# Kernel optimization log

Hardware: AMD Instinct MI355X
Metric: run time of the kernel (lower is better)

Reference implementation:

```python
import jax, jax.numpy as jnp
import numpy as np

K_TOP = 16
SPLITS = 16


def setup_inputs() -> dict:
    key = jax.random.key(0)
    kq, kt = jax.random.split(key)
    queries = jax.random.normal(kq, (4096, 128), dtype=jnp.float32)
    table = jax.random.normal(kt, (4096, 128, 128), dtype=jnp.float32)
    return {"queries": queries, "table": table}


def reference(queries, table):
    n_queries, vector_dim = queries.shape
    rows, scores_per_row, _ = table.shape
    table_size = rows * scores_per_row
    queries_per_split = n_queries // SPLITS
    q_split = queries.reshape(SPLITS, queries_per_split, vector_dim)
    row_offsets = jnp.arange(0, table_size, scores_per_row)  # [rows]

    def split_top_k(split_queries):
        # scores: [q, rows, values_per_row]
        split_scores = jnp.einsum('qd,rvd->qrv', split_queries, table)
        top_id_by_row = jnp.argmax(split_scores, axis=-1)        # [q, rows]
        top_score_by_row = jnp.max(split_scores, axis=-1)        # [q, rows]
        # top-k rows by per-row max score (descending)
        top_row_idx = jnp.argsort(top_score_by_row, axis=-1)[:, :-K_TOP - 1:-1]  # [q, k]
        # matmul_slice == gather along axis -1 (one-hot matmul trick on TPU)
        ids_by_topk_row = jnp.take_along_axis(top_id_by_row, top_row_idx, axis=-1)  # [q, k]
        split_topk_values = table[top_row_idx, ids_by_topk_row]  # [q, k, d]
        top_table_id_by_row = top_id_by_row + row_offsets        # [q, rows]
        split_topk_ids = jnp.take_along_axis(top_table_id_by_row, top_row_idx, axis=-1)
        split_topk_scores = jnp.take_along_axis(top_score_by_row, top_row_idx, axis=-1)
        return split_topk_values, split_topk_scores, split_topk_ids

    topk_values, topk_scores, topk_ids = jax.lax.map(split_top_k, q_split)
    topk_values = topk_values.reshape(n_queries, K_TOP, -1)
    topk_scores = topk_scores.reshape(n_queries, K_TOP)
    topk_ids = topk_ids.reshape(n_queries, K_TOP)
    return topk_values, topk_scores, topk_ids
```

## Files before the change

kernel.cpp:

```cpp
#include <hip/hip_runtime.h>
#include <stdint.h>


typedef __attribute__((ext_vector_type(8))) short short8;
typedef __attribute__((ext_vector_type(4))) float floatx4;
typedef __attribute__((ext_vector_type(16))) float floatx16;
typedef unsigned long long u64;
typedef unsigned int u32;

#define NQ 4096
#define NR 4096
#define NV 128
#define ND 128
#define KTOP 16
#define RC 16
#define NCHUNK (NR / RC)
#define CPC 8
#define CSEL 24
#define BCAP 1024

__device__ __forceinline__ unsigned short f2bf(float f) {
  u32 u = __float_as_uint(f);
  u32 r = u + 0x7FFFu + ((u >> 16) & 1u);
  return (unsigned short)(r >> 16);
}
__device__ __forceinline__ u32 key_of(float s) {
  u32 b = __float_as_uint(s);
  return (b & 0x80000000u) ? ~b : (b | 0x80000000u);
}
__device__ __forceinline__ float unkey(u32 k) {
  u32 b = (k & 0x80000000u) ? (k & 0x7FFFFFFFu) : ~k;
  return __uint_as_float(b);
}
__device__ __forceinline__ void glds16(const void* g, void* l) {
  __builtin_amdgcn_global_load_lds(
      (const __attribute__((address_space(1))) unsigned int*)g,
      (__attribute__((address_space(3))) unsigned int*)l, 16, 0, 0);
}

__global__ void k0_convert(const float* __restrict__ t, unsigned short* __restrict__ o) {
  size_t i = ((size_t)blockIdx.x * 256 + threadIdx.x) * 4;
  float4 v = *reinterpret_cast<const float4*>(t + i);
  ushort4 r;
  r.x = f2bf(v.x); r.y = f2bf(v.y); r.z = f2bf(v.z); r.w = f2bf(v.w);
  *reinterpret_cast<ushort4*>(o + i) = r;
}

__launch_bounds__(256, 2)
__global__ void k1_coarse(const float* __restrict__ Q, const unsigned short* __restrict__ T16,
                          u64* __restrict__ cand) {
  __shared__ short Blds[2][128 * 128];

  const int tid = threadIdx.x;
  const int wave = tid >> 6;
  const int lane = tid & 63;
  const int l31 = lane & 31;
  const int l15 = lane & 15;
  const int half = lane >> 5;
  const int qblock = blockIdx.x;
  const int chunk = blockIdx.y;

  short8 bfrag[8];
  {
    const float* qp = Q + (size_t)(qblock * 128 + wave * 32 + l31) * 128;
#pragma unroll
    for (int kb = 0; kb < 8; kb++) {
      float4 x = *reinterpret_cast<const float4*>(qp + kb * 16 + half * 8);
      float4 y = *reinterpret_cast<const float4*>(qp + kb * 16 + half * 8 + 4);
      short8 b;
      b[0] = (short)f2bf(x.x); b[1] = (short)f2bf(x.y);
      b[2] = (short)f2bf(x.z); b[3] = (short)f2bf(x.w);
      b[4] = (short)f2bf(y.x); b[5] = (short)f2bf(y.y);
      b[6] = (short)f2bf(y.z); b[7] = (short)f2bf(y.w);
      bfrag[kb] = b;
    }
  }

  int goff[8];
#pragma unroll
  for (int i = 0; i < 8; i++) {
    int v = wave * 32 + i * 4 + (lane >> 4);
    int kb = l15 ^ (v & 15);
    goff[i] = v * 256 + kb * 16;
  }
  const char* chunkbase = (const char*)(T16 + (size_t)(chunk * RC) * (NV * ND));

#pragma unroll
  for (int i = 0; i < 8; i++)
    glds16(chunkbase + goff[i], &Blds[0][(wave * 8 + i) * 512 + lane * 8]);
  __syncthreads();

  u64 a[CPC];
#pragma unroll
  for (int i = 0; i < CPC; i++) a[i] = 0;

  const short* abase = &Blds[0][l31 * 128];
  for (int rl = 0; rl < RC; rl++) {
    const int cur = rl & 1;
    if (rl < RC - 1) {
      const char* rs = chunkbase + (size_t)(rl + 1) * 32768;
#pragma unroll
      for (int i = 0; i < 8; i++)
        glds16(rs + goff[i], &Blds[1 - cur][(wave * 8 + i) * 512 + lane * 8]);
    }

    float run = -3.402823466e+38f;
#pragma unroll
    for (int t = 0; t < 4; t++) {
      floatx16 acc = 0;
#pragma unroll
      for (int kb = 0; kb < 8; kb++) {
        const short* ap = abase + cur * 16384 + t * 4096 +
                          8 * ((kb * 2 + half) ^ (l31 & 15));
        short8 af = *reinterpret_cast<const short8*>(ap);
        acc = __builtin_amdgcn_mfma_f32_32x32x16_bf16(af, bfrag[kb], acc, 0, 0, 0);
      }
      float m = acc[0];
#pragma unroll
      for (int r = 1; r < 16; r++) m = fmaxf(m, acc[r]);
      run = fmaxf(run, m);
    }
    run = fmaxf(run, __shfl_xor(run, 32, 64));

    u64 x = ((u64)key_of(run) << 32) | (u32)(chunk * RC + rl);
    if (x > a[CPC - 1]) {
#pragma unroll
      for (int p = 0; p < CPC; p++) {
        u64 mx = a[p] > x ? a[p] : x;
        u64 mn = a[p] > x ? x : a[p];
        a[p] = mx; x = mn;
      }
    }
    __syncthreads();
  }

  if (lane < 32) {
    const int q = qblock * 128 + wave * 32 + l31;
    u64* dst = cand + (size_t)q * (NCHUNK * CPC) + chunk * CPC;
#pragma unroll
    for (int i = 0; i < CPC; i++) dst[i] = a[i];
  }
}

__global__ void k2_select(const u64* __restrict__ cand, u64* __restrict__ refined,
                          u32* __restrict__ cnt, u32* __restrict__ bucket) {
  const int q = blockIdx.x;
  const int lane = threadIdx.x;
  const u64* base = cand + (size_t)q * (NCHUNK * CPC);
  u64 a[12];
#pragma unroll
  for (int i = 0; i < 12; i++) a[i] = 0;
  for (int i = 0; i < 32; i++) {
    u64 x = base[i * 64 + lane];
    if (x > a[11]) {
#pragma unroll
      for (int p = 0; p < 12; p++) {
        u64 mx = a[p] > x ? a[p] : x;
        u64 mn = a[p] > x ? x : a[p];
        a[p] = mx; x = mn;
      }
    }
  }
  if (lane < CSEL) refined[(size_t)q * CSEL + lane] = 0;

  for (int j = 0; j < CSEL; j++) {
    u64 head = a[0];
    u64 W = head;
#pragma unroll
    for (int off = 1; off < 64; off <<= 1) {
      u64 o = __shfl_xor(W, off, 64);
      if (o > W) W = o;
    }
    if (head == W) {
#pragma unroll
      for (int p = 0; p < 11; p++) a[p] = a[p + 1];
      a[11] = 0;
      u32 row = (u32)W & 4095u;
      u32 slot = atomicAdd(cnt + row, 1u);
      if (slot < BCAP) bucket[(size_t)row * BCAP + slot] = ((u32)q << 5) | (u32)j;
    }
  }
}

__global__ void k3_refine(const float* __restrict__ Q, const float* __restrict__ table,
                          const u32* __restrict__ cnt, const u32* __restrict__ bucket,
                          u64* __restrict__ refined) {
  __shared__ float rowv[128 * 128];
  const int row = blockIdx.x;
  const int tid = threadIdx.x;
  u32 n = cnt[row];
  if (n > BCAP) n = BCAP;
  if (n == 0) return;
  const float* src = table + (size_t)row * (NV * ND);
#pragma unroll
  for (int i = 0; i < 8; i++) {
    int idx = i * 2048 + tid * 4;
    int v = idx >> 7;
    int d4 = tid & 31;
    *reinterpret_cast<float4*>(&rowv[v * 128 + ((d4 ^ (v & 31)) << 2)]) =
        *reinterpret_cast<const float4*>(src + idx);
  }
  __syncthreads();
  const int v = tid & 127;
  const int lane = tid & 63;
  const int sw = v & 31;
  for (u32 ei = (u32)(tid >> 7); ei < n; ei += 4) {
    u32 ent = __builtin_amdgcn_readfirstlane(bucket[(size_t)row * BCAP + ei]);
    u32 q = ent >> 5, j = ent & 31u;
    const float* qp = Q + (size_t)q * 128;
    float acc = 0.f;
#pragma unroll
    for (int d4 = 0; d4 < 32; d4++) {
      float4 rv = *reinterpret_cast<const float4*>(&rowv[v * 128 + ((d4 ^ sw) << 2)]);
      acc = fmaf(rv.x, qp[d4 * 4 + 0], acc);
      acc = fmaf(rv.y, qp[d4 * 4 + 1], acc);
      acc = fmaf(rv.z, qp[d4 * 4 + 2], acc);
      acc = fmaf(rv.w, qp[d4 * 4 + 3], acc);
    }
    u64 p = ((u64)key_of(acc) << 32) | (u32)(127 - v);
#pragma unroll
    for (int off = 1; off < 64; off <<= 1) {
      u64 o = __shfl_xor(p, off, 64);
      if (o > p) p = o;
    }
    if (lane == 0) {
      u32 vbest = 127u - (u32)(p & 0xFFFFFFFFu);
      u64 packed = ((p >> 32) << 32) | (u32)(row * 128 + vbest);
      atomicMax(reinterpret_cast<unsigned long long*>(&refined[(size_t)q * CSEL + j]), packed);
    }
  }
}

__global__ void k4_finalize(const float* __restrict__ table, const u64* __restrict__ refined,
                            float* __restrict__ out) {
  __shared__ u64 arr[CSEL];
  __shared__ u32 fids[KTOP];
  __shared__ float scs[KTOP];
  const int q = blockIdx.x;
  const int tid = threadIdx.x;
  if (tid < CSEL) arr[tid] = refined[(size_t)q * CSEL + tid];
  __syncthreads();
  if (tid == 0) {
    for (int i = 1; i < CSEL; i++) {
      u64 x = arr[i]; int p = i;
      while (p > 0 && arr[p - 1] < x) { arr[p] = arr[p - 1]; p--; }
      arr[p] = x;
    }
    for (int i = 0; i < KTOP; i++) {
      fids[i] = (u32)arr[i];
      scs[i] = unkey((u32)(arr[i] >> 32));
    }
  }
  __syncthreads();
  const int i = tid >> 4, sub = tid & 15;
  const float* src = table + (size_t)fids[i] * 128 + sub * 8;
  float* dst = out + ((size_t)q * KTOP + i) * 128 + sub * 8;
  *reinterpret_cast<float4*>(dst) = *reinterpret_cast<const float4*>(src);
  *reinterpret_cast<float4*>(dst + 4) = *reinterpret_cast<const float4*>(src + 4);
  if (tid < KTOP) {
    out[8388608 + (size_t)q * KTOP + tid] = scs[tid];
    out[8388608 + 65536 + (size_t)q * KTOP + tid] = (float)fids[tid];
  }
}

extern "C" void kernel_launch(void* const* d_in, const int* in_sizes, int n_in,
                              void* d_out, int out_size, void* d_ws, size_t ws_size,
                              hipStream_t stream) {
  (void)in_sizes; (void)n_in; (void)out_size; (void)ws_size;
  const float* Q = (const float*)d_in[0];
  const float* T = (const float*)d_in[1];
  float* out = (float*)d_out;
  char* ws = (char*)d_ws;
  unsigned short* T16 = (unsigned short*)ws;
  u64* cand    = (u64*)(ws + 134217728);
  u32* cnt     = (u32*)(ws + 134217728 + 67108864);
  u32* bucket  = (u32*)(ws + 134217728 + 67108864 + 16384);
  u64* refined = (u64*)(ws + 134217728 + 67108864 + 16384 + 16777216);

  hipMemsetAsync(cnt, 0, NR * sizeof(u32), stream);
  k0_convert<<<65536, 256, 0, stream>>>(T, T16);
  k1_coarse<<<dim3(32, 256), 256, 0, stream>>>(Q, T16, cand);
  k2_select<<<NQ, 64, 0, stream>>>(cand, refined, cnt, bucket);
  k3_refine<<<NR, 512, 0, stream>>>(Q, T, cnt, bucket, refined);
  k4_finalize<<<NQ, 256, 0, stream>>>(T, refined, out);
}
```

Before: 1.211 ms.

## Double queries per wave in coarse kernel and batch four entries in refine

```diff
diff --git a/kernel.cpp b/kernel.cpp
--- a/kernel.cpp
+++ b/kernel.cpp
@@ -37,6 +37,23 @@
       (const __attribute__((address_space(1))) unsigned int*)g,
       (__attribute__((address_space(3))) unsigned int*)l, 16, 0, 0);
 }
+__device__ __forceinline__ float max16(floatx16 a) {
+  float m0 = fmaxf(fmaxf(a[0], a[1]), fmaxf(a[2], a[3]));
+  float m1 = fmaxf(fmaxf(a[4], a[5]), fmaxf(a[6], a[7]));
+  float m2 = fmaxf(fmaxf(a[8], a[9]), fmaxf(a[10], a[11]));
+  float m3 = fmaxf(fmaxf(a[12], a[13]), fmaxf(a[14], a[15]));
+  return fmaxf(fmaxf(m0, m1), fmaxf(m2, m3));
+}
+__device__ __forceinline__ void insert8(u64* a, u64 x) {
+  if (x > a[CPC - 1]) {
+#pragma unroll
+    for (int p = 0; p < CPC; p++) {
+      u64 mx = a[p] > x ? a[p] : x;
+      u64 mn = a[p] > x ? x : a[p];
+      a[p] = mx; x = mn;
+    }
+  }
+}
 
 __global__ void k0_convert(const float* __restrict__ t, unsigned short* __restrict__ o) {
   size_t i = ((size_t)blockIdx.x * 256 + threadIdx.x) * 4;
@@ -60,19 +77,27 @@
   const int qblock = blockIdx.x;
   const int chunk = blockIdx.y;
 
-  short8 bfrag[8];
+  short8 bf0[8], bf1[8];
   {
-    const float* qp = Q + (size_t)(qblock * 128 + wave * 32 + l31) * 128;
+    const float* qp0 = Q + (size_t)(qblock * 256 + wave * 64 + l31) * 128;
+    const float* qp1 = qp0 + 32 * 128;
 #pragma unroll
     for (int kb = 0; kb < 8; kb++) {
-      float4 x = *reinterpret_cast<const float4*>(qp + kb * 16 + half * 8);
-      float4 y = *reinterpret_cast<const float4*>(qp + kb * 16 + half * 8 + 4);
+      float4 x = *reinterpret_cast<const float4*>(qp0 + kb * 16 + half * 8);
+      float4 y = *reinterpret_cast<const float4*>(qp0 + kb * 16 + half * 8 + 4);
       short8 b;
       b[0] = (short)f2bf(x.x); b[1] = (short)f2bf(x.y);
       b[2] = (short)f2bf(x.z); b[3] = (short)f2bf(x.w);
       b[4] = (short)f2bf(y.x); b[5] = (short)f2bf(y.y);
       b[6] = (short)f2bf(y.z); b[7] = (short)f2bf(y.w);
-      bfrag[kb] = b;
+      bf0[kb] = b;
+      x = *reinterpret_cast<const float4*>(qp1 + kb * 16 + half * 8);
+      y = *reinterpret_cast<const float4*>(qp1 + kb * 16 + half * 8 + 4);
+      b[0] = (short)f2bf(x.x); b[1] = (short)f2bf(x.y);
+      b[2] = (short)f2bf(x.z); b[3] = (short)f2bf(x.w);
+      b[4] = (short)f2bf(y.x); b[5] = (short)f2bf(y.y);
+      b[6] = (short)f2bf(y.z); b[7] = (short)f2bf(y.w);
+      bf1[kb] = b;
     }
   }
 
@@ -90,9 +115,9 @@
     glds16(chunkbase + goff[i], &Blds[0][(wave * 8 + i) * 512 + lane * 8]);
   __syncthreads();
 
-  u64 a[CPC];
-#pragma unroll
-  for (int i = 0; i < CPC; i++) a[i] = 0;
+  u64 a0[CPC], a1[CPC];
+#pragma unroll
+  for (int i = 0; i < CPC; i++) { a0[i] = 0; a1[i] = 0; }
 
   const short* abase = &Blds[0][l31 * 128];
   for (int rl = 0; rl < RC; rl++) {
@@ -104,41 +129,36 @@
         glds16(rs + goff[i], &Blds[1 - cur][(wave * 8 + i) * 512 + lane * 8]);
     }
 
-    float run = -3.402823466e+38f;
+    float run0 = -3.402823466e+38f, run1 = -3.402823466e+38f;
 #pragma unroll
     for (int t = 0; t < 4; t++) {
-      floatx16 acc = 0;
+      floatx16 acc0 = 0, acc1 = 0;
 #pragma unroll
       for (int kb = 0; kb < 8; kb++) {
         const short* ap = abase + cur * 16384 + t * 4096 +
                           8 * ((kb * 2 + half) ^ (l31 & 15));
         short8 af = *reinterpret_cast<const short8*>(ap);
-        acc = __builtin_amdgcn_mfma_f32_32x32x16_bf16(af, bfrag[kb], acc, 0, 0, 0);
+        acc0 = __builtin_amdgcn_mfma_f32_32x32x16_bf16(af, bf0[kb], acc0, 0, 0, 0);
+        acc1 = __builtin_amdgcn_mfma_f32_32x32x16_bf16(af, bf1[kb], acc1, 0, 0, 0);
       }
-      float m = acc[0];
-#pragma unroll
-      for (int r = 1; r < 16; r++) m = fmaxf(m, acc[r]);
-      run = fmaxf(run, m);
-    }
-    run = fmaxf(run, __shfl_xor(run, 32, 64));
-
-    u64 x = ((u64)key_of(run) << 32) | (u32)(chunk * RC + rl);
-    if (x > a[CPC - 1]) {
-#pragma unroll
-      for (int p = 0; p < CPC; p++) {
-        u64 mx = a[p] > x ? a[p] : x;
-        u64 mn = a[p] > x ? x : a[p];
-        a[p] = mx; x = mn;
-      }
-    }
+      run0 = fmaxf(run0, max16(acc0));
+      run1 = fmaxf(run1, max16(acc1));
+    }
+    run0 = fmaxf(run0, __shfl_xor(run0, 32, 64));
+    run1 = fmaxf(run1, __shfl_xor(run1, 32, 64));
+
+    u32 rid = (u32)(chunk * RC + rl);
+    insert8(a0, ((u64)key_of(run0) << 32) | rid);
+    insert8(a1, ((u64)key_of(run1) << 32) | rid);
     __syncthreads();
   }
 
   if (lane < 32) {
-    const int q = qblock * 128 + wave * 32 + l31;
-    u64* dst = cand + (size_t)q * (NCHUNK * CPC) + chunk * CPC;
-#pragma unroll
-    for (int i = 0; i < CPC; i++) dst[i] = a[i];
+    const int q0 = qblock * 256 + wave * 64 + l31;
+    u64* dst0 = cand + (size_t)q0 * (NCHUNK * CPC) + chunk * CPC;
+    u64* dst1 = dst0 + (size_t)32 * (NCHUNK * CPC);
+#pragma unroll
+    for (int i = 0; i < CPC; i++) { dst0[i] = a0[i]; dst1[i] = a1[i]; }
   }
 }
 
@@ -179,6 +199,22 @@
       u32 slot = atomicAdd(cnt + row, 1u);
       if (slot < BCAP) bucket[(size_t)row * BCAP + slot] = ((u32)q << 5) | (u32)j;
     }
+  }
+}
+
+__device__ __forceinline__ void k3_emit(float acc, u32 ent, int row, int v, int lane,
+                                        u64* __restrict__ refined) {
+  u64 p = ((u64)key_of(acc) << 32) | (u32)(127 - v);
+#pragma unroll
+  for (int off = 1; off < 64; off <<= 1) {
+    u64 o = __shfl_xor(p, off, 64);
+    if (o > p) p = o;
+  }
+  if (lane == 0) {
+    u32 q = ent >> 5, j = ent & 31u;
+    u32 vbest = 127u - (u32)(p & 0xFFFFFFFFu);
+    u64 packed = ((p >> 32) << 32) | (u32)(row * 128 + vbest);
+    atomicMax(reinterpret_cast<unsigned long long*>(&refined[(size_t)q * CSEL + j]), packed);
   }
 }
 
@@ -193,41 +229,53 @@
   if (n == 0) return;
   const float* src = table + (size_t)row * (NV * ND);
 #pragma unroll
-  for (int i = 0; i < 8; i++) {
-    int idx = i * 2048 + tid * 4;
+  for (int i = 0; i < 16; i++) {
+    int idx = i * 1024 + tid * 4;
     int v = idx >> 7;
     int d4 = tid & 31;
     *reinterpret_cast<float4*>(&rowv[v * 128 + ((d4 ^ (v & 31)) << 2)]) =
         *reinterpret_cast<const float4*>(src + idx);
   }
   __syncthreads();
+  const int g = tid >> 7;
   const int v = tid & 127;
   const int lane = tid & 63;
   const int sw = v & 31;
-  for (u32 ei = (u32)(tid >> 7); ei < n; ei += 4) {
-    u32 ent = __builtin_amdgcn_readfirstlane(bucket[(size_t)row * BCAP + ei]);
-    u32 q = ent >> 5, j = ent & 31u;
-    const float* qp = Q + (size_t)q * 128;
-    float acc = 0.f;
+  const u32* bk = bucket + (size_t)row * BCAP;
+  for (u32 e0 = (u32)(g * 4); e0 < n; e0 += 8) {
+    u32 ent0 = __builtin_amdgcn_readfirstlane(bk[e0]);
+    u32 ent1 = __builtin_amdgcn_readfirstlane(bk[e0 + 1 < n ? e0 + 1 : e0]);
+    u32 ent2 = __builtin_amdgcn_readfirstlane(bk[e0 + 2 < n ? e0 + 2 : e0]);
+    u32 ent3 = __builtin_amdgcn_readfirstlane(bk[e0 + 3 < n ? e0 + 3 : e0]);
+    const float* qp0 = Q + (size_t)(ent0 >> 5) * 128;
+    const float* qp1 = Q + (size_t)(ent1 >> 5) * 128;
+    const float* qp2 = Q + (size_t)(ent2 >> 5) * 128;
+    const float* qp3 = Q + (size_t)(ent3 >> 5) * 128;
+    float c0 = 0.f, c1 = 0.f, c2 = 0.f, c3 = 0.f;
 #pragma unroll
     for (int d4 = 0; d4 < 32; d4++) {
       float4 rv = *reinterpret_cast<const float4*>(&rowv[v * 128 + ((d4 ^ sw) << 2)]);
-      acc = fmaf(rv.x, qp[d4 * 4 + 0], acc);
-      acc = fmaf(rv.y, qp[d4 * 4 + 1], acc);
-      acc = fmaf(rv.z, qp[d4 * 4 + 2], acc);
-      acc = fmaf(rv.w, qp[d4 * 4 + 3], acc);
-    }
-    u64 p = ((u64)key_of(acc) << 32) | (u32)(127 - v);
-#pragma unroll
-    for (int off = 1; off < 64; off <<= 1) {
-      u64 o = __shfl_xor(p, off, 64);
-      if (o > p) p = o;
-    }
-    if (lane == 0) {
-      u32 vbest = 127u - (u32)(p & 0xFFFFFFFFu);
-      u64 packed = ((p >> 32) << 32) | (u32)(row * 128 + vbest);
-      atomicMax(reinterpret_cast<unsigned long long*>(&refined[(size_t)q * CSEL + j]), packed);
-    }
+      c0 = fmaf(rv.x, qp0[d4 * 4 + 0], c0);
+      c0 = fmaf(rv.y, qp0[d4 * 4 + 1], c0);
+      c0 = fmaf(rv.z, qp0[d4 * 4 + 2], c0);
+      c0 = fmaf(rv.w, qp0[d4 * 4 + 3], c0);
+      c1 = fmaf(rv.x, qp1[d4 * 4 + 0], c1);
+      c1 = fmaf(rv.y, qp1[d4 * 4 + 1], c1);
+      c1 = fmaf(rv.z, qp1[d4 * 4 + 2], c1);
+      c1 = fmaf(rv.w, qp1[d4 * 4 + 3], c1);
+      c2 = fmaf(rv.x, qp2[d4 * 4 + 0], c2);
+      c2 = fmaf(rv.y, qp2[d4 * 4 + 1], c2);
+      c2 = fmaf(rv.z, qp2[d4 * 4 + 2], c2);
+      c2 = fmaf(rv.w, qp2[d4 * 4 + 3], c2);
+      c3 = fmaf(rv.x, qp3[d4 * 4 + 0], c3);
+      c3 = fmaf(rv.y, qp3[d4 * 4 + 1], c3);
+      c3 = fmaf(rv.z, qp3[d4 * 4 + 2], c3);
+      c3 = fmaf(rv.w, qp3[d4 * 4 + 3], c3);
+    }
+    k3_emit(c0, ent0, row, v, lane, refined);
+    if (e0 + 1 < n) k3_emit(c1, ent1, row, v, lane, refined);
+    if (e0 + 2 < n) k3_emit(c2, ent2, row, v, lane, refined);
+    if (e0 + 3 < n) k3_emit(c3, ent3, row, v, lane, refined);
   }
 }
 
@@ -279,8 +327,8 @@
 
   hipMemsetAsync(cnt, 0, NR * sizeof(u32), stream);
   k0_convert<<<65536, 256, 0, stream>>>(T, T16);
-  k1_coarse<<<dim3(32, 256), 256, 0, stream>>>(Q, T16, cand);
+  k1_coarse<<<dim3(16, 256), 256, 0, stream>>>(Q, T16, cand);
   k2_select<<<NQ, 64, 0, stream>>>(cand, refined, cnt, bucket);
-  k3_refine<<<NR, 512, 0, stream>>>(Q, T, cnt, bucket, refined);
+  k3_refine<<<NR, 256, 0, stream>>>(Q, T, cnt, bucket, refined);
   k4_finalize<<<NQ, 256, 0, stream>>>(T, refined, out);
 }
```

New measurement: 1.316 ms. +8.6%, slower.
